# Kernel tuning notes

Measured on AMD Instinct MI355X. Metric: run time of the kernel, lower is better.

## Reference

```python
import jax, jax.numpy as jnp
import numpy as np

B, L, E, D, A = 256, 196, 2048, 1024, 512


def setup_inputs() -> dict:
    key = jax.random.key(0)
    ks = jax.random.split(key, 9)
    enc_scale = 1.0 / np.sqrt(E)
    dec_scale = 1.0 / np.sqrt(D)
    att_scale = 1.0 / np.sqrt(A)
    return {
        "encoder_out": jax.random.normal(ks[0], (B, L, E), dtype=jnp.float32),
        "decoder_hidden": jax.random.normal(ks[1], (B, D), dtype=jnp.float32),
        "mask1": jax.random.randint(ks[2], (B, L), 0, 2, dtype=jnp.int32),
        "We": jax.random.uniform(ks[3], (E, A), jnp.float32, -enc_scale, enc_scale),
        "be": jax.random.uniform(ks[4], (A,), jnp.float32, -enc_scale, enc_scale),
        "Wd": jax.random.uniform(ks[5], (D, A), jnp.float32, -dec_scale, dec_scale),
        "bd": jax.random.uniform(ks[6], (A,), jnp.float32, -dec_scale, dec_scale),
        "wf": jax.random.uniform(ks[7], (A,), jnp.float32, -att_scale, att_scale),
        "bf": jax.random.uniform(ks[8], (), jnp.float32, -att_scale, att_scale),
    }


def reference(encoder_out, decoder_hidden, mask1, We, be, Wd, bd, wf, bf):
    # att1: [B, L, A]; att2: [B, A]
    att1 = jnp.einsum('ble,ea->bla', encoder_out, We) + be
    att2 = jnp.einsum('bd,da->ba', decoder_hidden, Wd) + bd
    # scores: [B, L]
    att = jnp.einsum('bla,a->bl', jnp.tanh(att1 + att2[:, None, :]), wf) + bf
    att = jnp.where(mask1 == 0, jnp.float32(-1e9), att)
    alpha = jax.nn.softmax(att, axis=1)
    # weighted sum over regions: [B, E]
    awe = jnp.einsum('ble,bl->be', encoder_out, alpha)
    return (awe, alpha)
```

## Files before the change

kernel.cpp:

```cpp
#include <hip/hip_runtime.h>
#include <hip/hip_bf16.h>


#define B_ 256
#define L_ 196
#define E_ 2048
#define D_ 1024
#define A_ 512
#define M_TOT (B_ * L_)

typedef __attribute__((ext_vector_type(8))) short bf16x8;
typedef __attribute__((ext_vector_type(4))) float f32x4;

static __device__ __forceinline__ unsigned short f2bf(float f) {
    union { float f; unsigned u; } u{f};
    unsigned r = u.u + 0x7fffu + ((u.u >> 16) & 1u);
    return (unsigned short)(r >> 16);
}

__global__ __launch_bounds__(256) void k_wepack(const float* __restrict__ We,
                                                unsigned short* __restrict__ WeP) {
    int i = blockIdx.x * 256 + threadIdx.x;
    int k = i >> 9, n = i & 511;
    WeP[((k >> 5) << 14) + (n << 5) + (k & 31)] = f2bf(We[i]);
}

__global__ __launch_bounds__(256) void k_bias2(const float* __restrict__ dec,
                                               const float* __restrict__ Wd,
                                               const float* __restrict__ be,
                                               const float* __restrict__ bd,
                                               float* __restrict__ bias2) {
    int b = blockIdx.x, t = threadIdx.x;
    __shared__ float ds[D_];
    for (int i = t; i < D_; i += 256) ds[i] = dec[b * D_ + i];
    __syncthreads();
    for (int a0 = 0; a0 < A_; a0 += 256) {
        int a = a0 + t;
        float acc = 0.f;
        #pragma unroll 8
        for (int d = 0; d < D_; d++) acc += ds[d] * Wd[d * A_ + a];
        bias2[b * A_ + a] = acc + be[a] + bd[a];
    }
}

__global__ __launch_bounds__(512) void k_gemm_score(
        const float* __restrict__ enc,
        const unsigned short* __restrict__ WeP,
        const float* __restrict__ bias2,
        const float* __restrict__ wf,
        float* __restrict__ scores) {
    __shared__ __align__(16) unsigned short a_lds[64 * 48];
    __shared__ __align__(16) unsigned short b_lds[512 * 48];
    __shared__ float score_lds[64];

    const int tid = threadIdx.x;
    const int m0 = blockIdx.x * 64;
    const int lane = tid & 63;
    const int wid = tid >> 6;
    const int wm = wid >> 2, wn = wid & 3;
    const int kg = lane >> 4, lr = lane & 15;

    const int ar = tid >> 3;
    const int akc = (tid & 7) << 2;
    const float* aptr = enc + (size_t)(m0 + ar) * E_ + akc;
    const unsigned short* bptr = WeP + ((size_t)tid << 5);

    f32x4 acc[2][8];
    #pragma unroll
    for (int i = 0; i < 2; i++)
        #pragma unroll
        for (int j = 0; j < 8; j++) acc[i][j] = (f32x4){0.f, 0.f, 0.f, 0.f};

    for (int kb = 0; kb < 64; kb++) {
        float4 av = *reinterpret_cast<const float4*>(aptr + kb * 32);
        short4 ap;
        ap.x = (short)f2bf(av.x); ap.y = (short)f2bf(av.y);
        ap.z = (short)f2bf(av.z); ap.w = (short)f2bf(av.w);
        *reinterpret_cast<short4*>(&a_lds[ar * 48 + akc]) = ap;
        const uint4* bsrc = reinterpret_cast<const uint4*>(bptr + ((size_t)kb << 14));
        uint4 b0 = bsrc[0], b1 = bsrc[1], b2 = bsrc[2], b3 = bsrc[3];
        uint4* bdst = reinterpret_cast<uint4*>(&b_lds[tid * 48]);
        bdst[0] = b0; bdst[1] = b1; bdst[2] = b2; bdst[3] = b3;
        __syncthreads();

        bf16x8 af[2];
        #pragma unroll
        for (int i = 0; i < 2; i++)
            af[i] = *reinterpret_cast<const bf16x8*>(
                &a_lds[(wm * 32 + i * 16 + lr) * 48 + kg * 8]);
        bf16x8 bfr[8];
        #pragma unroll
        for (int j = 0; j < 8; j++)
            bfr[j] = *reinterpret_cast<const bf16x8*>(
                &b_lds[(wn * 128 + j * 16 + lr) * 48 + kg * 8]);
        #pragma unroll
        for (int i = 0; i < 2; i++)
            #pragma unroll
            for (int j = 0; j < 8; j++)
                acc[i][j] = __builtin_amdgcn_mfma_f32_16x16x32_bf16(
                    af[i], bfr[j], acc[i][j], 0, 0, 0);
        __syncthreads();
    }

    if (tid < 64) score_lds[tid] = 0.f;
    __syncthreads();
    #pragma unroll
    for (int i = 0; i < 2; i++) {
        #pragma unroll
        for (int r = 0; r < 4; r++) {
            int R = wm * 32 + i * 16 + kg * 4 + r;
            int gm = m0 + R;
            int bg = gm / L_;
            float sum = 0.f;
            #pragma unroll
            for (int j = 0; j < 8; j++) {
                int C = wn * 128 + j * 16 + lr;
                float x = acc[i][j][r] + bias2[bg * A_ + C];
                sum += wf[C] * tanhf(x);
            }
            #pragma unroll
            for (int mk = 1; mk < 16; mk <<= 1) sum += __shfl_xor(sum, mk);
            if (lr == 0) atomicAdd(&score_lds[R], sum);
        }
    }
    __syncthreads();
    if (tid < 64) scores[m0 + tid] = score_lds[tid];
}

__global__ __launch_bounds__(256) void k_softmax(const float* __restrict__ scores,
                                                 const int* __restrict__ mask,
                                                 const float* __restrict__ bfp,
                                                 float* __restrict__ alpha) {
    int b = blockIdx.x, t = threadIdx.x;
    float bfv = bfp[0];
    float v = -INFINITY;
    if (t < L_) v = (mask[b * L_ + t] == 0) ? -1e9f : (scores[b * L_ + t] + bfv);
    __shared__ float redm[4], reds[4];
    float m = v;
    #pragma unroll
    for (int s = 1; s < 64; s <<= 1) m = fmaxf(m, __shfl_xor(m, s));
    int w = t >> 6;
    if ((t & 63) == 0) redm[w] = m;
    __syncthreads();
    m = fmaxf(fmaxf(redm[0], redm[1]), fmaxf(redm[2], redm[3]));
    float e = (t < L_) ? expf(v - m) : 0.f;
    float s = e;
    #pragma unroll
    for (int k = 1; k < 64; k <<= 1) s += __shfl_xor(s, k);
    if ((t & 63) == 0) reds[w] = s;
    __syncthreads();
    s = reds[0] + reds[1] + reds[2] + reds[3];
    if (t < L_) alpha[b * L_ + t] = e / s;
}

__global__ __launch_bounds__(64) void k_awe(const float* __restrict__ enc,
                                            const float* __restrict__ alpha,
                                            float* __restrict__ awe) {
    int b = blockIdx.y, ec = blockIdx.x, t = threadIdx.x;
    __shared__ float al[L_];
    for (int l = t; l < L_; l += 64) al[l] = alpha[b * L_ + l];
    __syncthreads();
    int e0 = (ec << 8) + (t << 2);
    const float* base = enc + (size_t)b * L_ * E_ + e0;
    float4 acc = {0.f, 0.f, 0.f, 0.f};
    #pragma unroll 4
    for (int l = 0; l < L_; l++) {
        float4 v = *reinterpret_cast<const float4*>(base + (size_t)l * E_);
        float a = al[l];
        acc.x += a * v.x; acc.y += a * v.y; acc.z += a * v.z; acc.w += a * v.w;
    }
    *reinterpret_cast<float4*>(awe + b * E_ + e0) = acc;
}

extern "C" void kernel_launch(void* const* d_in, const int* in_sizes, int n_in,
                              void* d_out, int out_size, void* d_ws, size_t ws_size,
                              hipStream_t stream) {
    const float* enc  = (const float*)d_in[0];
    const float* dec  = (const float*)d_in[1];
    const int*   mask = (const int*)d_in[2];
    const float* We   = (const float*)d_in[3];
    const float* be   = (const float*)d_in[4];
    const float* Wd   = (const float*)d_in[5];
    const float* bd   = (const float*)d_in[6];
    const float* wf   = (const float*)d_in[7];
    const float* bf   = (const float*)d_in[8];

    float* awe   = (float*)d_out;
    float* alpha = awe + (size_t)B_ * E_;

    char* ws = (char*)d_ws;
    unsigned short* WeP = (unsigned short*)ws;
    float* bias2  = (float*)(ws + (2u << 20));
    float* scores = (float*)(ws + (2u << 20) + (512u << 10));

    hipLaunchKernelGGL(k_wepack, dim3((E_ * A_) / 256), dim3(256), 0, stream, We, WeP);
    hipLaunchKernelGGL(k_bias2, dim3(B_), dim3(256), 0, stream, dec, Wd, be, bd, bias2);
    hipLaunchKernelGGL(k_gemm_score, dim3(M_TOT / 64), dim3(512), 0, stream,
                       enc, WeP, bias2, wf, scores);
    hipLaunchKernelGGL(k_softmax, dim3(B_), dim3(256), 0, stream, scores, mask, bf, alpha);
    hipLaunchKernelGGL(k_awe, dim3(8, B_), dim3(64), 0, stream, enc, alpha, awe);
}
```

Before: 458.9 us.

## Load GEMM operands directly into registers, drop LDS staging and barriers

The score GEMM no longer stages encoder and weight tiles through shared memory. Each lane loads its MFMA fragments straight from global memory into registers, with A prefetched two k-steps ahead and B one step ahead, so both __syncthreads per k-step go away. Occupancy is raised with launch_bounds(512,3), and tanhf is replaced by an exp/reciprocal formula. The cost is redundant global loads: A rows are re-read by each of the 4 wn waves and B by both wm waves, so L2 traffic rises, register pressure grows, and the fast tanh gives up some accuracy.

```diff
diff --git a/kernel.cpp b/kernel.cpp
--- a/kernel.cpp
+++ b/kernel.cpp
@@ -43,14 +43,12 @@
     }
 }
 
-__global__ __launch_bounds__(512) void k_gemm_score(
+__global__ __launch_bounds__(512, 3) void k_gemm_score(
         const float* __restrict__ enc,
         const unsigned short* __restrict__ WeP,
         const float* __restrict__ bias2,
         const float* __restrict__ wf,
         float* __restrict__ scores) {
-    __shared__ __align__(16) unsigned short a_lds[64 * 48];
-    __shared__ __align__(16) unsigned short b_lds[512 * 48];
     __shared__ float score_lds[64];
 
     const int tid = threadIdx.x;
@@ -60,10 +58,9 @@
     const int wm = wid >> 2, wn = wid & 3;
     const int kg = lane >> 4, lr = lane & 15;
 
-    const int ar = tid >> 3;
-    const int akc = (tid & 7) << 2;
-    const float* aptr = enc + (size_t)(m0 + ar) * E_ + akc;
-    const unsigned short* bptr = WeP + ((size_t)tid << 5);
+    const float* aP0 = enc + (size_t)(m0 + wm * 32 + lr) * E_ + kg * 8;
+    const float* aP1 = aP0 + 16 * E_;
+    const unsigned short* bP = WeP + (wn * 128 + lr) * 32 + kg * 8;
 
     f32x4 acc[2][8];
     #pragma unroll
@@ -71,35 +68,57 @@
         #pragma unroll
         for (int j = 0; j < 8; j++) acc[i][j] = (f32x4){0.f, 0.f, 0.f, 0.f};
 
-    for (int kb = 0; kb < 64; kb++) {
-        float4 av = *reinterpret_cast<const float4*>(aptr + kb * 32);
-        short4 ap;
-        ap.x = (short)f2bf(av.x); ap.y = (short)f2bf(av.y);
-        ap.z = (short)f2bf(av.z); ap.w = (short)f2bf(av.w);
-        *reinterpret_cast<short4*>(&a_lds[ar * 48 + akc]) = ap;
-        const uint4* bsrc = reinterpret_cast<const uint4*>(bptr + ((size_t)kb << 14));
-        uint4 b0 = bsrc[0], b1 = bsrc[1], b2 = bsrc[2], b3 = bsrc[3];
-        uint4* bdst = reinterpret_cast<uint4*>(&b_lds[tid * 48]);
-        bdst[0] = b0; bdst[1] = b1; bdst[2] = b2; bdst[3] = b3;
-        __syncthreads();
-
+    float4 a0[2][2], a1[2][2];
+    bf16x8 bR[8];
+
+    #pragma unroll
+    for (int i = 0; i < 2; i++) {
+        const float* p = (i ? aP1 : aP0);
+        a0[i][0] = *reinterpret_cast<const float4*>(p);
+        a0[i][1] = *reinterpret_cast<const float4*>(p + 4);
+        a1[i][0] = *reinterpret_cast<const float4*>(p + 32);
+        a1[i][1] = *reinterpret_cast<const float4*>(p + 36);
+    }
+    #pragma unroll
+    for (int j = 0; j < 8; j++)
+        bR[j] = *reinterpret_cast<const bf16x8*>(bP + j * 512);
+
+    auto phase = [&](float4 (&aC)[2][2], int tc) {
         bf16x8 af[2];
         #pragma unroll
-        for (int i = 0; i < 2; i++)
-            af[i] = *reinterpret_cast<const bf16x8*>(
-                &a_lds[(wm * 32 + i * 16 + lr) * 48 + kg * 8]);
-        bf16x8 bfr[8];
-        #pragma unroll
-        for (int j = 0; j < 8; j++)
-            bfr[j] = *reinterpret_cast<const bf16x8*>(
-                &b_lds[(wn * 128 + j * 16 + lr) * 48 + kg * 8]);
+        for (int i = 0; i < 2; i++) {
+            union { bf16x8 v; unsigned short s[8]; } u;
+            u.s[0] = f2bf(aC[i][0].x); u.s[1] = f2bf(aC[i][0].y);
+            u.s[2] = f2bf(aC[i][0].z); u.s[3] = f2bf(aC[i][0].w);
+            u.s[4] = f2bf(aC[i][1].x); u.s[5] = f2bf(aC[i][1].y);
+            u.s[6] = f2bf(aC[i][1].z); u.s[7] = f2bf(aC[i][1].w);
+            af[i] = u.v;
+        }
+        if (tc + 2 < 64) {
+            #pragma unroll
+            for (int i = 0; i < 2; i++) {
+                const float* p = (i ? aP1 : aP0) + (tc + 2) * 32;
+                aC[i][0] = *reinterpret_cast<const float4*>(p);
+                aC[i][1] = *reinterpret_cast<const float4*>(p + 4);
+            }
+        }
         #pragma unroll
         for (int i = 0; i < 2; i++)
             #pragma unroll
             for (int j = 0; j < 8; j++)
                 acc[i][j] = __builtin_amdgcn_mfma_f32_16x16x32_bf16(
-                    af[i], bfr[j], acc[i][j], 0, 0, 0);
-        __syncthreads();
+                    af[i], bR[j], acc[i][j], 0, 0, 0);
+        if (tc + 1 < 64) {
+            const unsigned short* bp = bP + (size_t)(tc + 1) * 16384;
+            #pragma unroll
+            for (int j = 0; j < 8; j++)
+                bR[j] = *reinterpret_cast<const bf16x8*>(bp + j * 512);
+        }
+    };
+
+    for (int t = 0; t < 64; t += 2) {
+        phase(a0, t);
+        phase(a1, t + 1);
     }
 
     if (tid < 64) score_lds[tid] = 0.f;
@@ -116,7 +135,9 @@
             for (int j = 0; j < 8; j++) {
                 int C = wn * 128 + j * 16 + lr;
                 float x = acc[i][j][r] + bias2[bg * A_ + C];
-                sum += wf[C] * tanhf(x);
+                float ex = __expf(2.f * x);
+                float th = 1.f - 2.f * __builtin_amdgcn_rcpf(ex + 1.f);
+                sum += wf[C] * th;
             }
             #pragma unroll
             for (int mk = 1; mk < 16; mk <<= 1) sum += __shfl_xor(sum, mk);
```

Result: slower. 682.9 us (+48.8%).
